# Performance work log

Hardware: AMD Instinct MI355X
Metric: run time of the kernel (lower is better)

Reference implementation:

```python
import jax, jax.numpy as jnp
import numpy as np

H_DIM = 64
GRID = 8
NBR = 2.0
BN_EPS = 1e-5
N_SEQ = 64
N_PED = 64
BOTTLENECK = 1024


def setup_inputs() -> dict:
    key = jax.random.key(0)
    k0, k1, k2, k3 = jax.random.split(key, 4)
    batch = N_SEQ * N_PED
    h_states = jax.random.normal(k0, (1, batch, H_DIM), jnp.float32)
    # positions spread over a 4x4 area so some neighbors fall inside the 2.0 neighborhood
    end_pos = jax.random.uniform(k1, (batch, 2), jnp.float32) * 4.0
    rel_pos = jax.random.normal(k2, (batch, 2), jnp.float32)
    starts = jnp.arange(N_SEQ, dtype=jnp.int32) * N_PED
    seq_start_end = jnp.stack([starts, starts + N_PED], axis=1)
    in_dim = GRID * GRID * H_DIM  # 4096
    W = jax.random.normal(k3, (in_dim, BOTTLENECK), jnp.float32) / np.sqrt(in_dim)
    b = jnp.zeros((BOTTLENECK,), jnp.float32)
    gamma = jnp.ones((BOTTLENECK,), jnp.float32)
    beta = jnp.zeros((BOTTLENECK,), jnp.float32)
    return {"h_states": h_states, "seq_start_end": seq_start_end, "end_pos": end_pos,
            "rel_pos": rel_pos, "W": W, "b": b, "gamma": gamma, "beta": beta}


def _pool_scene(hidden, pos):
    # hidden: (n, h), pos: (n, 2). Pair (i, j): ped j binned into ped i's grid.
    n, h = hidden.shape
    g2 = GRID * GRID
    half = NBR / 2.0
    tl_x = pos[:, 0] - half
    tl_y = pos[:, 1] + half
    br_x = pos[:, 0] + half
    br_y = pos[:, 1] - half
    px = pos[None, :, 0]  # (1, n) -> broadcast over i
    py = pos[None, :, 1]
    cell_x = jnp.floor((px - tl_x[:, None]) / NBR * GRID)
    cell_y = jnp.floor((tl_y[:, None] - py) / NBR * GRID)
    grid = (cell_x + cell_y * GRID).astype(jnp.int32) + 1  # slot 0 = trash bin
    oob = ((px >= br_x[:, None]) | (px <= tl_x[:, None]) |
           (py >= tl_y[:, None]) | (py <= br_y[:, None]) |
           jnp.eye(n, dtype=bool))  # self-interaction excluded
    grid = grid + (jnp.arange(n, dtype=jnp.int32) * g2)[:, None]
    grid = jnp.where(oob, 0, grid)  # (n, n)
    src = jnp.broadcast_to(hidden[None], (n, n, h)).reshape(-1, h)
    buf = jnp.zeros((n * g2 + 1, h), hidden.dtype).at[grid.reshape(-1)].add(src)
    return buf[1:].reshape(n, g2 * h)


def reference(h_states, seq_start_end, end_pos, rel_pos, W, b, gamma, beta):
    batch = end_pos.shape[0]
    n_seq = seq_start_end.shape[0]
    n_ped = batch // n_seq  # equal-length scenes by construction
    hid = h_states.reshape(-1, H_DIM).reshape(n_seq, n_ped, H_DIM)
    pos = end_pos.reshape(n_seq, n_ped, 2)
    pool_h = jax.vmap(_pool_scene)(hid, pos).reshape(batch, -1)  # (batch, 4096)
    x = pool_h @ W + b
    # BatchNorm1d in training mode (batch statistics, biased variance)
    mean = jnp.mean(x, axis=0)
    var = jnp.var(x, axis=0)
    x = (x - mean) * jax.lax.rsqrt(var + BN_EPS) * gamma + beta
    return jax.nn.relu(x)
```

## Files before the change

### kernel.cpp

```cpp
#include <hip/hip_runtime.h>
#include <hip/hip_bf16.h>


#define NPED  64
#define BATCH 4096
#define HDIM  64
#define G2    64
#define KDIM  4096
#define NOUT  1024

typedef __attribute__((ext_vector_type(8))) short short8;
typedef __attribute__((ext_vector_type(4))) float f32x4;

__device__ __forceinline__ unsigned short f2bf(float f) {
    __hip_bfloat16 h = __float2bfloat16(f);
    return *reinterpret_cast<unsigned short*>(&h);
}

__global__ __launch_bounds__(512) void pool_kernel(const float* __restrict__ h,
                                                   const float* __restrict__ pos,
                                                   unsigned short* __restrict__ A2) {
    __shared__ float hs[NPED * HDIM];
    __shared__ float pl[NPED * 2];
    int t = threadIdx.x;
    int w = t >> 6, lane = t & 63;
    int p0 = blockIdx.x * 8;
    int sbase = p0 & ~(NPED - 1);
    if (t < 128) pl[t] = pos[sbase * 2 + t];
    {
        const float4* src = (const float4*)(h + (size_t)sbase * HDIM);
        float4* dst = (float4*)hs;
        dst[t] = src[t];
        dst[t + 512] = src[t + 512];
    }
    __syncthreads();

    int i = p0 + w;
    int il = i & (NPED - 1);
    float cx0 = pl[2 * il], cy0 = pl[2 * il + 1];
    float tlx = cx0 - 1.f, tly = cy0 + 1.f, brx = cx0 + 1.f, bry = cy0 - 1.f;
    float px = pl[2 * lane], py = pl[2 * lane + 1];
    bool inb = (lane != il) && !(px >= brx || px <= tlx || py >= tly || py <= bry);
    int cellx = (int)floorf((px - tlx) * 4.f);
    int celly = (int)floorf((tly - py) * 4.f);
    int cell = cellx + celly * 8;
    inb = inb && ((unsigned)cell < 64u);

    int mtile = i >> 4, r = i & 15;
    unsigned short* outb = A2 + (size_t)mtile * 65536 + r * 8
                              + (lane >> 5) * 512 + ((lane >> 3) & 3) * 128 + (lane & 7);
    const float* hrow = hs + lane;
    #pragma unroll
    for (int c = 0; c < 64; ++c) {
        unsigned long long m = __ballot(inb && (cell == c));
        float a = 0.f;
        while (m) {
            int j = __builtin_ctzll(m);
            m &= m - 1;
            a += hrow[j * HDIM];
        }
        outb[c * 1024] = f2bf(a);
    }
}

__global__ __launch_bounds__(256) void wt_kernel(const float* __restrict__ W,
                                                 unsigned short* __restrict__ Wt2,
                                                 float* __restrict__ stats) {
    __shared__ unsigned short tile[64][66];
    int k0 = blockIdx.x * 64;
    int n0 = blockIdx.y * 64;
    int t = threadIdx.x;
    if (blockIdx.x == 0 && blockIdx.y < 8) stats[blockIdx.y * 256 + t] = 0.f;
    #pragma unroll
    for (int p = 0; p < 4; ++p) {
        int lin = p * 256 + t;
        int c4 = lin & 15, kl = lin >> 4;
        float4 v = ((const float4*)(W + (size_t)(k0 + kl) * NOUT + n0))[c4];
        tile[c4 * 4 + 0][kl] = f2bf(v.x);
        tile[c4 * 4 + 1][kl] = f2bf(v.y);
        tile[c4 * 4 + 2][kl] = f2bf(v.z);
        tile[c4 * 4 + 3][kl] = f2bf(v.w);
    }
    __syncthreads();
    unsigned int* out = (unsigned int*)Wt2;
    #pragma unroll
    for (int p = 0; p < 8; ++p) {
        int lin = p * 256 + t;
        int qq = lin & 3;
        int r = (lin >> 2) & 15;
        int chunk = (lin >> 6) & 3;
        int ktl = (lin >> 8) & 1;
        int ntl = lin >> 9;
        int nl = ntl * 16 + r;
        int kl = ktl * 32 + chunk * 8 + qq * 2;
        unsigned int v = (unsigned int)tile[nl][kl] |
                         ((unsigned int)tile[nl][kl + 1] << 16);
        out[(size_t)(blockIdx.y * 4 + ntl) * 32768 + (size_t)(blockIdx.x * 2 + ktl) * 256
            + chunk * 64 + r * 4 + qq] = v;
    }
}

__global__ __launch_bounds__(128) void gemm_kernel(const unsigned short* __restrict__ A2,
                                                   const unsigned short* __restrict__ Wt2,
                                                   float* __restrict__ C,
                                                   float* __restrict__ P1) {
    int t = threadIdx.x;
    int w = t >> 6, lane = t & 63;
    int mtile0 = blockIdx.x * 16 + w * 8;
    int ntile0 = blockIdx.y * 4;
    int ktile0 = blockIdx.z * 64;

    f32x4 acc[8][4];
    #pragma unroll
    for (int i = 0; i < 8; ++i)
        #pragma unroll
        for (int j = 0; j < 4; ++j)
            acc[i][j] = (f32x4){0.f, 0.f, 0.f, 0.f};

    const unsigned short* Ab = A2 + (size_t)mtile0 * 65536 + (size_t)ktile0 * 512 + lane * 8;
    const unsigned short* Bb = Wt2 + (size_t)ntile0 * 65536 + (size_t)ktile0 * 512 + lane * 8;

    short8 a_c[8], b_c[4], a_n[8], b_n[4];
    #pragma unroll
    for (int i = 0; i < 8; ++i) a_c[i] = *(const short8*)(Ab + (size_t)i * 65536);
    #pragma unroll
    for (int j = 0; j < 4; ++j) b_c[j] = *(const short8*)(Bb + (size_t)j * 65536);

    #pragma unroll 2
    for (int kt = 0; kt < 64; ++kt) {
        if (kt < 63) {
            const unsigned short* An = Ab + (size_t)(kt + 1) * 512;
            const unsigned short* Bn = Bb + (size_t)(kt + 1) * 512;
            #pragma unroll
            for (int i = 0; i < 8; ++i) a_n[i] = *(const short8*)(An + (size_t)i * 65536);
            #pragma unroll
            for (int j = 0; j < 4; ++j) b_n[j] = *(const short8*)(Bn + (size_t)j * 65536);
        }
        #pragma unroll
        for (int j = 0; j < 4; ++j)
            #pragma unroll
            for (int i = 0; i < 8; ++i)
                acc[i][j] = __builtin_amdgcn_mfma_f32_16x16x32_bf16(a_c[i], b_c[j], acc[i][j], 0, 0, 0);
        #pragma unroll
        for (int i = 0; i < 8; ++i) a_c[i] = a_n[i];
        #pragma unroll
        for (int j = 0; j < 4; ++j) b_c[j] = b_n[j];
    }

    float* dst = blockIdx.z ? P1 : C;
    int row0 = mtile0 * 16 + ((lane >> 4) << 2);
    int col0 = ntile0 * 16 + (lane & 15);
    #pragma unroll
    for (int i = 0; i < 8; ++i)
        #pragma unroll
        for (int j = 0; j < 4; ++j)
            #pragma unroll
            for (int r = 0; r < 4; ++r)
                dst[(size_t)(row0 + i * 16 + r) * NOUT + col0 + j * 16] = acc[i][j][r];
}

__global__ __launch_bounds__(256) void combine_stats(float* __restrict__ C,
                                                     const float* __restrict__ P1,
                                                     float* __restrict__ stats) {
    int t = threadIdx.x;
    int colchunk = blockIdx.x & 3;
    int rowchunk = blockIdx.x >> 2;
    int col = colchunk * 256 + t;
    size_t base = (size_t)rowchunk * 32 * NOUT + col;
    float s = 0.f, s2 = 0.f;
    #pragma unroll 4
    for (int r = 0; r < 32; ++r) {
        size_t ix = base + (size_t)r * NOUT;
        float v = C[ix] + P1[ix];
        C[ix] = v;
        s += v; s2 += v * v;
    }
    atomicAdd(&stats[col], s);
    atomicAdd(&stats[NOUT + col], s2);
}

__global__ __launch_bounds__(256) void norm_kernel(float* __restrict__ C,
                                                   const float* __restrict__ stats,
                                                   const float* __restrict__ gamma,
                                                   const float* __restrict__ beta) {
    int idx = blockIdx.x * 256 + threadIdx.x;
    int col4 = idx & 255;
    float4 x = ((const float4*)C)[idx];
    float4 s = ((const float4*)stats)[col4];
    float4 q = ((const float4*)(stats + NOUT))[col4];
    float4 g = ((const float4*)gamma)[col4];
    float4 b = ((const float4*)beta)[col4];
    const float inv_n = 1.f / 4096.f;
    float m, inv;
    m = s.x * inv_n; inv = rsqrtf(q.x * inv_n - m * m + 1e-5f); x.x = fmaxf((x.x - m) * inv * g.x + b.x, 0.f);
    m = s.y * inv_n; inv = rsqrtf(q.y * inv_n - m * m + 1e-5f); x.y = fmaxf((x.y - m) * inv * g.y + b.y, 0.f);
    m = s.z * inv_n; inv = rsqrtf(q.z * inv_n - m * m + 1e-5f); x.z = fmaxf((x.z - m) * inv * g.z + b.z, 0.f);
    m = s.w * inv_n; inv = rsqrtf(q.w * inv_n - m * m + 1e-5f); x.w = fmaxf((x.w - m) * inv * g.w + b.w, 0.f);
    ((float4*)C)[idx] = x;
}

extern "C" void kernel_launch(void* const* d_in, const int* in_sizes, int n_in,
                              void* d_out, int out_size, void* d_ws, size_t ws_size,
                              hipStream_t stream) {
    const float* h      = (const float*)d_in[0];
    const float* endpos = (const float*)d_in[2];
    const float* W      = (const float*)d_in[4];
    const float* gamma  = (const float*)d_in[6];
    const float* beta   = (const float*)d_in[7];
    float* C = (float*)d_out;

    char* ws = (char*)d_ws;
    size_t off = 0;
    unsigned short* A2  = (unsigned short*)(ws + off); off += (size_t)BATCH * KDIM * 2;
    unsigned short* Wt2 = (unsigned short*)(ws + off); off += (size_t)NOUT * KDIM * 2;
    float* P1 = (float*)(ws + off); off += (size_t)BATCH * NOUT * 4;
    float* stats = (float*)(ws + off);

    pool_kernel<<<BATCH / 8, 512, 0, stream>>>(h, endpos, A2);
    wt_kernel<<<dim3(KDIM / 64, NOUT / 64), 256, 0, stream>>>(W, Wt2, stats);
    gemm_kernel<<<dim3(16, 16, 2), 128, 0, stream>>>(A2, Wt2, C, P1);
    combine_stats<<<512, 256, 0, stream>>>(C, P1, stats);
    norm_kernel<<<(BATCH * NOUT / 4) / 256, 256, 0, stream>>>(C, stats, gamma, beta);
}
```

Measured before the change: 160.2 us.

## Raise GEMM split-K to four and use 2x2 wave tiling per block

The GEMM goes from 2-way to 4-way split-K and uses 256-thread blocks whose four waves each own a 4x4 tile grid in a 2x2 arrangement. Per-wave accumulators drop from 8x4 to 4x4, which cuts register pressure, and the launch grows from 512 to 1024 blocks for better occupancy. The prefetch is rewritten as explicit ping-pong double buffering. The cost is two extra 16 MB fp32 partial buffers that the GEMM must write and combine_stats must read back, adding substantial memory traffic.

```diff
diff --git a/kernel.cpp b/kernel.cpp
--- a/kernel.cpp
+++ b/kernel.cpp
@@ -100,19 +100,21 @@
     }
 }
 
-__global__ __launch_bounds__(128) void gemm_kernel(const unsigned short* __restrict__ A2,
+__global__ __launch_bounds__(256) void gemm_kernel(const unsigned short* __restrict__ A2,
                                                    const unsigned short* __restrict__ Wt2,
                                                    float* __restrict__ C,
-                                                   float* __restrict__ P1) {
+                                                   float* __restrict__ P1,
+                                                   float* __restrict__ P2,
+                                                   float* __restrict__ P3) {
     int t = threadIdx.x;
     int w = t >> 6, lane = t & 63;
-    int mtile0 = blockIdx.x * 16 + w * 8;
-    int ntile0 = blockIdx.y * 4;
-    int ktile0 = blockIdx.z * 64;
-
-    f32x4 acc[8][4];
-    #pragma unroll
-    for (int i = 0; i < 8; ++i)
+    int mtile0 = blockIdx.x * 8 + (w >> 1) * 4;
+    int ntile0 = blockIdx.y * 8 + (w & 1) * 4;
+    int ktile0 = blockIdx.z * 32;
+
+    f32x4 acc[4][4];
+    #pragma unroll
+    for (int i = 0; i < 4; ++i)
         #pragma unroll
         for (int j = 0; j < 4; ++j)
             acc[i][j] = (f32x4){0.f, 0.f, 0.f, 0.f};
@@ -120,38 +122,45 @@
     const unsigned short* Ab = A2 + (size_t)mtile0 * 65536 + (size_t)ktile0 * 512 + lane * 8;
     const unsigned short* Bb = Wt2 + (size_t)ntile0 * 65536 + (size_t)ktile0 * 512 + lane * 8;
 
-    short8 a_c[8], b_c[4], a_n[8], b_n[4];
-    #pragma unroll
-    for (int i = 0; i < 8; ++i) a_c[i] = *(const short8*)(Ab + (size_t)i * 65536);
-    #pragma unroll
-    for (int j = 0; j < 4; ++j) b_c[j] = *(const short8*)(Bb + (size_t)j * 65536);
-
-    #pragma unroll 2
-    for (int kt = 0; kt < 64; ++kt) {
-        if (kt < 63) {
-            const unsigned short* An = Ab + (size_t)(kt + 1) * 512;
-            const unsigned short* Bn = Bb + (size_t)(kt + 1) * 512;
-            #pragma unroll
-            for (int i = 0; i < 8; ++i) a_n[i] = *(const short8*)(An + (size_t)i * 65536);
-            #pragma unroll
-            for (int j = 0; j < 4; ++j) b_n[j] = *(const short8*)(Bn + (size_t)j * 65536);
+    short8 a0[4], b0[4], a1[4], b1[4];
+    #pragma unroll
+    for (int i = 0; i < 4; ++i) {
+        a0[i] = *(const short8*)(Ab + (size_t)i * 65536);
+        b0[i] = *(const short8*)(Bb + (size_t)i * 65536);
+    }
+
+    for (int kt = 0; kt < 32; kt += 2) {
+        if (kt + 1 < 32) {
+            #pragma unroll
+            for (int i = 0; i < 4; ++i) {
+                a1[i] = *(const short8*)(Ab + (size_t)i * 65536 + (kt + 1) * 512);
+                b1[i] = *(const short8*)(Bb + (size_t)i * 65536 + (kt + 1) * 512);
+            }
         }
         #pragma unroll
         for (int j = 0; j < 4; ++j)
             #pragma unroll
-            for (int i = 0; i < 8; ++i)
-                acc[i][j] = __builtin_amdgcn_mfma_f32_16x16x32_bf16(a_c[i], b_c[j], acc[i][j], 0, 0, 0);
-        #pragma unroll
-        for (int i = 0; i < 8; ++i) a_c[i] = a_n[i];
-        #pragma unroll
-        for (int j = 0; j < 4; ++j) b_c[j] = b_n[j];
-    }
-
-    float* dst = blockIdx.z ? P1 : C;
+            for (int i = 0; i < 4; ++i)
+                acc[i][j] = __builtin_amdgcn_mfma_f32_16x16x32_bf16(a0[i], b0[j], acc[i][j], 0, 0, 0);
+        if (kt + 2 < 32) {
+            #pragma unroll
+            for (int i = 0; i < 4; ++i) {
+                a0[i] = *(const short8*)(Ab + (size_t)i * 65536 + (kt + 2) * 512);
+                b0[i] = *(const short8*)(Bb + (size_t)i * 65536 + (kt + 2) * 512);
+            }
+        }
+        #pragma unroll
+        for (int j = 0; j < 4; ++j)
+            #pragma unroll
+            for (int i = 0; i < 4; ++i)
+                acc[i][j] = __builtin_amdgcn_mfma_f32_16x16x32_bf16(a1[i], b1[j], acc[i][j], 0, 0, 0);
+    }
+
+    float* dst = blockIdx.z == 0 ? C : blockIdx.z == 1 ? P1 : blockIdx.z == 2 ? P2 : P3;
     int row0 = mtile0 * 16 + ((lane >> 4) << 2);
     int col0 = ntile0 * 16 + (lane & 15);
     #pragma unroll
-    for (int i = 0; i < 8; ++i)
+    for (int i = 0; i < 4; ++i)
         #pragma unroll
         for (int j = 0; j < 4; ++j)
             #pragma unroll
@@ -161,6 +170,8 @@
 
 __global__ __launch_bounds__(256) void combine_stats(float* __restrict__ C,
                                                      const float* __restrict__ P1,
+                                                     const float* __restrict__ P2,
+                                                     const float* __restrict__ P3,
                                                      float* __restrict__ stats) {
     int t = threadIdx.x;
     int colchunk = blockIdx.x & 3;
@@ -171,7 +182,7 @@
     #pragma unroll 4
     for (int r = 0; r < 32; ++r) {
         size_t ix = base + (size_t)r * NOUT;
-        float v = C[ix] + P1[ix];
+        float v = (C[ix] + P1[ix]) + (P2[ix] + P3[ix]);
         C[ix] = v;
         s += v; s2 += v * v;
     }
@@ -214,11 +225,13 @@
     unsigned short* A2  = (unsigned short*)(ws + off); off += (size_t)BATCH * KDIM * 2;
     unsigned short* Wt2 = (unsigned short*)(ws + off); off += (size_t)NOUT * KDIM * 2;
     float* P1 = (float*)(ws + off); off += (size_t)BATCH * NOUT * 4;
+    float* P2 = (float*)(ws + off); off += (size_t)BATCH * NOUT * 4;
+    float* P3 = (float*)(ws + off); off += (size_t)BATCH * NOUT * 4;
     float* stats = (float*)(ws + off);
 
     pool_kernel<<<BATCH / 8, 512, 0, stream>>>(h, endpos, A2);
     wt_kernel<<<dim3(KDIM / 64, NOUT / 64), 256, 0, stream>>>(W, Wt2, stats);
-    gemm_kernel<<<dim3(16, 16, 2), 128, 0, stream>>>(A2, Wt2, C, P1);
-    combine_stats<<<512, 256, 0, stream>>>(C, P1, stats);
+    gemm_kernel<<<dim3(32, 8, 4), 256, 0, stream>>>(A2, Wt2, C, P1, P2, P3);
+    combine_stats<<<512, 256, 0, stream>>>(C, P1, P2, P3, stats);
     norm_kernel<<<(BATCH * NOUT / 4) / 256, 256, 0, stream>>>(C, stats, gamma, beta);
 }
```

Result: slower. 163.9 us (+2.3%).
